# Performance work log

Hardware: AMD Instinct MI355X
Metric: run time of the kernel (lower is better)

Reference implementation:

```python
import jax, jax.numpy as jnp
import numpy as np


def log_g(x):
    # log of g(x) = relu(x)+0.5 for x>=0, sigmoid(x) for x<0 (continuous minGRU activation)
    return jnp.where(x >= 0, jnp.log(jax.nn.relu(x) + 0.5), -jax.nn.softplus(-x))


def parallel_scan_log(log_coeffs, log_values):
    # log_coeffs: [B,T,H], log_values: [B,T+1,H]
    a_star = jnp.pad(jnp.cumsum(log_coeffs, axis=1), ((0, 0), (1, 0), (0, 0)))  # [B,T+1,H]
    log_h = a_star + jax.lax.cumlogsumexp(log_values - a_star, axis=1)
    return jnp.exp(log_h)  # [B,T+1,H]


def setup_inputs() -> dict:
    key = jax.random.key(0)
    B, T, D, H = 8, 4096, 1024, 1024
    k1, k2, k3, k4, k5, k6 = jax.random.split(key, 6)
    scale = 1.0 / np.sqrt(D)
    return {
        "x": jax.random.normal(k1, (B, T, D), dtype=jnp.float32),
        "h_0": jax.random.uniform(k2, (B, 1, H), dtype=jnp.float32),
        "W_z": jax.random.uniform(k3, (H, D), minval=-scale, maxval=scale, dtype=jnp.float32),
        "b_z": jax.random.uniform(k4, (H,), minval=-scale, maxval=scale, dtype=jnp.float32),
        "W_h": jax.random.uniform(k5, (H, D), minval=-scale, maxval=scale, dtype=jnp.float32),
        "b_h": jax.random.uniform(k6, (H,), minval=-scale, maxval=scale, dtype=jnp.float32),
    }


def reference(x, h_0, W_z, b_z, W_h, b_h):
    # k = linear_z(x)
    k = jnp.einsum('btd,hd->bth', x, W_z) + b_z                 # [B,T,H]
    log_z = -jax.nn.softplus(-k)                                # log sigmoid(k)
    log_coeffs = -jax.nn.softplus(k)                            # log (1 - sigmoid(k))
    log_h_0 = log_g(h_0)                                        # [B,1,H]
    log_tilde_h = log_g(jnp.einsum('btd,hd->bth', x, W_h) + b_h)  # [B,T,H]
    log_values = jnp.concatenate([log_h_0, log_z + log_tilde_h], axis=1)  # [B,T+1,H]
    h = parallel_scan_log(log_coeffs, log_values)               # [B,T+1,H]
    return h
```

## Files before the change

kernel.cpp:

```cpp
#include <hip/hip_runtime.h>
#include <stdint.h>

#define B_ 8
#define T_ 4096
#define D_ 1024
#define H_ 1024
#define M_ (B_*T_)
#define K_ D_
#define N_ H_
#define TC 32
#define NC (T_/TC)

typedef short short8 __attribute__((ext_vector_type(8)));
typedef float f32x4 __attribute__((ext_vector_type(4)));
typedef unsigned short ushort8v __attribute__((ext_vector_type(8)));

__device__ __forceinline__ float bf2f(unsigned short u) {
    union { unsigned int i; float f; } x; x.i = ((unsigned int)u) << 16; return x.f;
}
__device__ __forceinline__ unsigned short f2bf(float f) {
    union { float f; unsigned int i; } x; x.f = f;
    unsigned int u = x.i;
    unsigned int r = u + 0x7fffu + ((u >> 16) & 1u);
    return (unsigned short)(r >> 16);
}
__device__ __forceinline__ void gld_lds16(const unsigned short* g, unsigned short* l) {
    __builtin_amdgcn_global_load_lds(
        (const __attribute__((address_space(1))) void*)(const void*)g,
        (__attribute__((address_space(3))) void*)(void*)l, 16, 0, 0);
}
__device__ __forceinline__ float gfun(float x) {
    return x >= 0.f ? x + 0.5f : 1.f / (1.f + __expf(-x));
}

__global__ void cvt_kernel(const float* __restrict__ src, unsigned short* __restrict__ dst, int n4) {
    int i = blockIdx.x * blockDim.x + threadIdx.x;
    const int stride = gridDim.x * blockDim.x;
    for (; i < n4; i += stride) {
        float4 v = ((const float4*)src)[i];
        ushort4 o;
        o.x = f2bf(v.x); o.y = f2bf(v.y); o.z = f2bf(v.z); o.w = f2bf(v.w);
        ((ushort4*)dst)[i] = o;
    }
}

__global__ void cvtw_kernel(const float* __restrict__ Wz, const float* __restrict__ Wh,
                            unsigned short* __restrict__ wzb, unsigned short* __restrict__ whb, int n4) {
    const float* src = blockIdx.y ? Wh : Wz;
    unsigned short* dst = blockIdx.y ? whb : wzb;
    int i = blockIdx.x * blockDim.x + threadIdx.x;
    const int stride = gridDim.x * blockDim.x;
    for (; i < n4; i += stride) {
        float4 v = ((const float4*)src)[i];
        ushort4 o;
        o.x = f2bf(v.x); o.y = f2bf(v.y); o.z = f2bf(v.z); o.w = f2bf(v.w);
        ((ushort4*)dst)[i] = o;
    }
}

#define SB() __builtin_amdgcn_sched_barrier(0)
#define BAR() do { SB(); __builtin_amdgcn_s_barrier(); SB(); } while (0)

__global__ __launch_bounds__(512, 2) void gemm_kernel(
    const unsigned short* __restrict__ Xb,
    const unsigned short* __restrict__ Wzb,
    const unsigned short* __restrict__ Whb,
    const float* __restrict__ bz, const float* __restrict__ bh,
    unsigned short* __restrict__ KzOut, unsigned short* __restrict__ KhOut)
{
    __shared__ __align__(16) unsigned short ldsA[2][256 * 64];
    __shared__ __align__(16) unsigned short ldsB[2][256 * 64];

    const int bx = blockIdx.x;
    const int bn = blockIdx.y;
    const int mat = blockIdx.z;
    const unsigned short* Wb = mat ? Whb : Wzb;
    const float* bias = mat ? bh : bz;
    unsigned short* Out = mat ? KhOut : KzOut;

    const int tid = threadIdx.x;
    const int w = tid >> 6, lane = tid & 63;
    const int wm = w >> 2, wn = w & 3;

    const int srow = lane >> 3;
    const int schunk = ((lane & 7) ^ srow) << 3;
    const unsigned short* gA = Xb + (size_t)(bx * 1024 + srow) * K_ + schunk;
    const unsigned short* gB = Wb + (size_t)(bn * 256 + srow) * K_ + schunk;

#define STAGE_A(s, g, h) do { \
    gld_lds16(gA + (size_t)(((g) >> 4) * 256 + (h)*128 + w*8) * K_ + ((g)&15) * 64, \
              &ldsA[s][((h)*128 + w*8) * 64]); \
    gld_lds16(gA + (size_t)(((g) >> 4) * 256 + (h)*128 + 64 + w*8) * K_ + ((g)&15) * 64, \
              &ldsA[s][((h)*128 + 64 + w*8) * 64]); \
  } while (0)
#define STAGE_B(s, g, h) do { \
    gld_lds16(gB + (size_t)((h)*128 + w*8) * K_ + ((g)&15) * 64, \
              &ldsB[s][((h)*128 + w*8) * 64]); \
    gld_lds16(gB + (size_t)((h)*128 + 64 + w*8) * K_ + ((g)&15) * 64, \
              &ldsB[s][((h)*128 + 64 + w*8) * 64]); \
  } while (0)

    const int lrow = lane & 15;
    const int q = lane >> 4;
    const int sw0 = (q ^ (lane & 7)) << 3;

#define LDA(s, fm, kh) (*(const short8*)&ldsA[s][(wm*128 + (fm)*16 + lrow) * 64 + (sw0 ^ ((kh)*32))])
#define LDB(s, fn, kh) (*(const short8*)&ldsB[s][(wn*64  + (fn)*16 + lrow) * 64 + (sw0 ^ ((kh)*32))])

#define RD_A4(s, fmb) do { \
    _Pragma("unroll") for (int f = 0; f < 4; ++f) { Ar[f][0] = LDA(s, (fmb)+f, 0); Ar[f][1] = LDA(s, (fmb)+f, 1); } \
  } while (0)
#define RD_B2(s, fnb) do { \
    _Pragma("unroll") for (int g2_ = 0; g2_ < 2; ++g2_) { Br[(fnb)+g2_][0] = LDB(s, (fnb)+g2_, 0); Br[(fnb)+g2_][1] = LDB(s, (fnb)+g2_, 1); } \
  } while (0)

#define QUAD(mb, nb) do { \
    __builtin_amdgcn_s_setprio(1); \
    _Pragma("unroll") for (int f = 0; f < 4; ++f) { \
      _Pragma("unroll") for (int g2_ = 0; g2_ < 2; ++g2_) { \
        acc[(mb)+f][(nb)+g2_] = __builtin_amdgcn_mfma_f32_16x16x32_bf16(Ar[f][0], Br[(nb)+g2_][0], acc[(mb)+f][(nb)+g2_], 0, 0, 0); \
        acc[(mb)+f][(nb)+g2_] = __builtin_amdgcn_mfma_f32_16x16x32_bf16(Ar[f][1], Br[(nb)+g2_][1], acc[(mb)+f][(nb)+g2_], 0, 0, 0); \
      } \
    } \
    __builtin_amdgcn_s_setprio(0); \
  } while (0)

    f32x4 acc[8][4];
    short8 Ar[4][2], Br[4][2];

    float bb[4];
#pragma unroll
    for (int fn = 0; fn < 4; ++fn) bb[fn] = bias[bn * 256 + wn * 64 + fn * 16 + lrow];

    STAGE_B(0, 0, 0); STAGE_B(0, 0, 1);
    STAGE_A(0, 0, 0); STAGE_A(0, 0, 1);
    STAGE_B(1, 1, 0); STAGE_B(1, 1, 1);
    SB();
    asm volatile("s_waitcnt vmcnt(4)" ::: "memory");
    BAR();

#pragma unroll 1
    for (int t = 0; t < 4; ++t) {
#pragma unroll
        for (int i = 0; i < 8; ++i)
#pragma unroll
            for (int j = 0; j < 4; ++j) acc[i][j] = (f32x4){0.f, 0.f, 0.f, 0.f};

#pragma unroll 1
        for (int i = 0; i < 8; ++i) {
            const int g1 = t * 16 + 2 * i + 1;
            const int g2 = g1 + 1;
            const int g3 = g1 + 2;
            const bool st = (g2 < 64);

            RD_A4(0, 0); RD_B2(0, 0);
            STAGE_A(1, g1, 0);
            BAR();
            QUAD(0, 0);
            BAR();
            RD_B2(0, 2);
            STAGE_A(1, g1, 1);
            BAR();
            QUAD(0, 2);
            BAR();
            RD_A4(0, 4);
            if (st) STAGE_B(0, g2, 0);
            BAR();
            QUAD(4, 0);
            BAR();
            if (st) {
                STAGE_B(0, g2, 1);
                SB();
                asm volatile("s_waitcnt vmcnt(4)" ::: "memory");
            } else {
                asm volatile("s_waitcnt vmcnt(0)" ::: "memory");
            }
            BAR();
            QUAD(4, 2);
            BAR();
            RD_A4(1, 0); RD_B2(1, 0);
            if (st) STAGE_A(0, g2, 0);
            BAR();
            QUAD(0, 0);
            BAR();
            RD_B2(1, 2);
            if (st) STAGE_A(0, g2, 1);
            BAR();
            QUAD(0, 2);
            BAR();
            RD_A4(1, 4);
            if (st) STAGE_B(1, g3, 0);
            BAR();
            QUAD(4, 0);
            BAR();
            if (st) {
                STAGE_B(1, g3, 1);
                SB();
                asm volatile("s_waitcnt vmcnt(4)" ::: "memory");
            }
            BAR();
            QUAD(4, 2);
            BAR();
        }

#pragma unroll
        for (int fn = 0; fn < 4; ++fn) {
            const int n = bn * 256 + wn * 64 + fn * 16 + lrow;
#pragma unroll
            for (int fm = 0; fm < 8; ++fm) {
                const int mq = (bx * 4 + t) * 64 + wm * 32 + fm * 4 + q;
                ushort4 o;
                o.x = f2bf(acc[fm][fn][0] + bb[fn]);
                o.y = f2bf(acc[fm][fn][1] + bb[fn]);
                o.z = f2bf(acc[fm][fn][2] + bb[fn]);
                o.w = f2bf(acc[fm][fn][3] + bb[fn]);
                *(ushort4*)(Out + ((size_t)mq * N_ + n) * 4) = o;
            }
        }
    }
}


__global__ __launch_bounds__(256) void scanA_kernel(const unsigned short* __restrict__ Kz,
                                                    const unsigned short* __restrict__ Kh,
                                                    float* __restrict__ Fc, float* __restrict__ Vc)
{
    const int c = blockIdx.x, b = blockIdx.y;
    const int hb = threadIdx.x * 4;
    float F[4] = {1.f, 1.f, 1.f, 1.f}, V[4] = {0.f, 0.f, 0.f, 0.f};
    size_t base = ((size_t)(b * (T_ / 4) + c * (TC / 4)) * N_ + hb) * 4;
    for (int qq = 0; qq < TC / 4; qq++) {
        ushort8v z0 = *(const ushort8v*)(Kz + base);
        ushort8v z1 = *(const ushort8v*)(Kz + base + 8);
        ushort8v h0v = *(const ushort8v*)(Kh + base);
        ushort8v h1v = *(const ushort8v*)(Kh + base + 8);
        base += (size_t)N_ * 4;
#pragma unroll
        for (int r = 0; r < 4; r++) {
            float kzf[4] = {bf2f(z0[r]), bf2f(z0[4 + r]), bf2f(z1[r]), bf2f(z1[4 + r])};
            float khf[4] = {bf2f(h0v[r]), bf2f(h0v[4 + r]), bf2f(h1v[r]), bf2f(h1v[4 + r])};
#pragma unroll
            for (int j = 0; j < 4; j++) {
                float f = 1.f / (1.f + __expf(kzf[j]));
                float v = (1.f - f) * gfun(khf[j]);
                V[j] = f * V[j] + v;
                F[j] *= f;
            }
        }
    }
    size_t o = ((size_t)(b * NC + c)) * H_ + hb;
    *(float4*)(Fc + o) = make_float4(F[0], F[1], F[2], F[3]);
    *(float4*)(Vc + o) = make_float4(V[0], V[1], V[2], V[3]);
}

__global__ __launch_bounds__(64) void scanB_kernel(const float* __restrict__ h0,
                                                   const float* __restrict__ Fc,
                                                   const float* __restrict__ Vc,
                                                   float* __restrict__ Carry,
                                                   float* __restrict__ Out)
{
    const int b = blockIdx.x;
    const int h = blockIdx.y * 256 + threadIdx.x * 4;
    float cy[4];
#pragma unroll
    for (int j = 0; j < 4; j++) cy[j] = gfun(h0[(size_t)b * H_ + h + j]);
    *(float4*)(Out + (size_t)b * (T_ + 1) * H_ + h) = make_float4(cy[0], cy[1], cy[2], cy[3]);
    size_t o = ((size_t)(b * NC)) * H_ + h;
    float4 F4 = *(const float4*)(Fc + o);
    float4 V4 = *(const float4*)(Vc + o);
    for (int c = 0; c < NC; c++) {
        const size_t on = o + H_;
        float4 nF, nV;
        if (c + 1 < NC) {
            nF = *(const float4*)(Fc + on);
            nV = *(const float4*)(Vc + on);
        }
        *(float4*)(Carry + o) = make_float4(cy[0], cy[1], cy[2], cy[3]);
        cy[0] = F4.x * cy[0] + V4.x;
        cy[1] = F4.y * cy[1] + V4.y;
        cy[2] = F4.z * cy[2] + V4.z;
        cy[3] = F4.w * cy[3] + V4.w;
        F4 = nF; V4 = nV; o = on;
    }
}

__global__ __launch_bounds__(256) void scanC_kernel(const unsigned short* __restrict__ Kz,
                                                    const unsigned short* __restrict__ Kh,
                                                    const float* __restrict__ Carry,
                                                    float* __restrict__ Out)
{
    const int c = blockIdx.x, b = blockIdx.y;
    const int hb = threadIdx.x * 4;
    float cy[4];
    {
        float4 c4 = *(const float4*)(Carry + ((size_t)(b * NC + c)) * H_ + hb);
        cy[0] = c4.x; cy[1] = c4.y; cy[2] = c4.z; cy[3] = c4.w;
    }
    size_t base = ((size_t)(b * (T_ / 4) + c * (TC / 4)) * N_ + hb) * 4;
    size_t ob = ((size_t)(b * (T_ + 1) + c * TC + 1)) * H_ + hb;
    for (int qq = 0; qq < TC / 4; qq++) {
        ushort8v z0 = *(const ushort8v*)(Kz + base);
        ushort8v z1 = *(const ushort8v*)(Kz + base + 8);
        ushort8v h0v = *(const ushort8v*)(Kh + base);
        ushort8v h1v = *(const ushort8v*)(Kh + base + 8);
        base += (size_t)N_ * 4;
#pragma unroll
        for (int r = 0; r < 4; r++) {
            float kzf[4] = {bf2f(z0[r]), bf2f(z0[4 + r]), bf2f(z1[r]), bf2f(z1[4 + r])};
            float khf[4] = {bf2f(h0v[r]), bf2f(h0v[4 + r]), bf2f(h1v[r]), bf2f(h1v[4 + r])};
#pragma unroll
            for (int j = 0; j < 4; j++) {
                float f = 1.f / (1.f + __expf(kzf[j]));
                float v = (1.f - f) * gfun(khf[j]);
                cy[j] = f * cy[j] + v;
            }
            *(float4*)(Out + ob) = make_float4(cy[0], cy[1], cy[2], cy[3]);
            ob += H_;
        }
    }
}

extern "C" void kernel_launch(void* const* d_in, const int* in_sizes, int n_in,
                              void* d_out, int out_size, void* d_ws, size_t ws_size,
                              hipStream_t stream)
{
    const float* x  = (const float*)d_in[0];
    const float* h0 = (const float*)d_in[1];
    const float* Wz = (const float*)d_in[2];
    const float* bz = (const float*)d_in[3];
    const float* Wh = (const float*)d_in[4];
    const float* bh = (const float*)d_in[5];
    float* out = (float*)d_out;

    char* ws = (char*)d_ws;
    unsigned short* xb  = (unsigned short*)ws; ws += (size_t)M_ * K_ * 2;
    unsigned short* wzb = (unsigned short*)ws; ws += (size_t)N_ * K_ * 2;
    unsigned short* whb = (unsigned short*)ws; ws += (size_t)N_ * K_ * 2;
    unsigned short* kz  = (unsigned short*)ws; ws += (size_t)M_ * N_ * 2;
    unsigned short* kh  = (unsigned short*)ws; ws += (size_t)M_ * N_ * 2;
    float* Fc    = (float*)ws; ws += (size_t)B_ * NC * H_ * 4;
    float* Vc    = (float*)ws; ws += (size_t)B_ * NC * H_ * 4;
    float* Carry = (float*)ws; ws += (size_t)B_ * NC * H_ * 4;

    cvt_kernel<<<2048, 256, 0, stream>>>(x, xb, M_ * K_ / 4);
    cvtw_kernel<<<dim3(128, 2), 256, 0, stream>>>(Wz, Wh, wzb, whb, N_ * K_ / 4);

    dim3 gg(M_ / 1024, N_ / 256, 2);
    gemm_kernel<<<gg, 512, 0, stream>>>(xb, wzb, whb, bz, bh, kz, kh);

    scanA_kernel<<<dim3(NC, B_), 256, 0, stream>>>(kz, kh, Fc, Vc);
    scanB_kernel<<<dim3(B_, H_ / 256), 64, 0, stream>>>(h0, Fc, Vc, Carry, out);
    scanC_kernel<<<dim3(NC, B_), 256, 0, stream>>>(kz, kh, Carry, out);
}
```

Measured before the change: 459.7 us.

## Fuse three-pass chunked scan into single decoupled-lookback scan kernel

Replaces the separate chunk-reduce, serial carry, and chunk-apply scan kernels with one kernel using decoupled lookback. Each block publishes its aggregate and then its inclusive prefix through per-chunk flags, and spins on its predecessors. The chunk size is doubled, to 64. This removes two kernel launches and the slow serial carry kernel. In exchange it adds spin-wait synchronisation whose progress relies on lower block indices being scheduled first, plus a flag-clear launch.

```diff
diff --git a/kernel.cpp b/kernel.cpp
--- a/kernel.cpp
+++ b/kernel.cpp
@@ -8,8 +8,8 @@
 #define M_ (B_*T_)
 #define K_ D_
 #define N_ H_
-#define TC 32
-#define NC (T_/TC)
+#define TC2 64
+#define NC2 (T_/TC2)
 
 typedef short short8 __attribute__((ext_vector_type(8)));
 typedef float f32x4 __attribute__((ext_vector_type(4)));
@@ -58,6 +58,11 @@
     }
 }
 
+__global__ void clear_kernel(int* __restrict__ flags, int n) {
+    int i = blockIdx.x * blockDim.x + threadIdx.x;
+    if (i < n) flags[i] = 0;
+}
+
 #define SB() __builtin_amdgcn_sched_barrier(0)
 #define BAR() do { SB(); __builtin_amdgcn_s_barrier(); SB(); } while (0)
 
@@ -221,15 +226,20 @@
 }
 
 
-__global__ __launch_bounds__(256) void scanA_kernel(const unsigned short* __restrict__ Kz,
-                                                    const unsigned short* __restrict__ Kh,
-                                                    float* __restrict__ Fc, float* __restrict__ Vc)
+__global__ __launch_bounds__(256) void scan_fused(
+    const unsigned short* __restrict__ Kz, const unsigned short* __restrict__ Kh,
+    const float* __restrict__ h0,
+    float* __restrict__ FA, float* __restrict__ VA, float* __restrict__ Incl,
+    int* flags, float* __restrict__ Out)
 {
     const int c = blockIdx.x, b = blockIdx.y;
     const int hb = threadIdx.x * 4;
+    __shared__ int sh_flag;
+
     float F[4] = {1.f, 1.f, 1.f, 1.f}, V[4] = {0.f, 0.f, 0.f, 0.f};
-    size_t base = ((size_t)(b * (T_ / 4) + c * (TC / 4)) * N_ + hb) * 4;
-    for (int qq = 0; qq < TC / 4; qq++) {
+    const size_t base0 = ((size_t)(b * (T_ / 4) + c * (TC2 / 4)) * N_ + hb) * 4;
+    size_t base = base0;
+    for (int qq = 0; qq < TC2 / 4; qq++) {
         ushort8v z0 = *(const ushort8v*)(Kz + base);
         ushort8v z1 = *(const ushort8v*)(Kz + base + 8);
         ushort8v h0v = *(const ushort8v*)(Kh + base);
@@ -248,57 +258,73 @@
             }
         }
     }
-    size_t o = ((size_t)(b * NC + c)) * H_ + hb;
-    *(float4*)(Fc + o) = make_float4(F[0], F[1], F[2], F[3]);
-    *(float4*)(Vc + o) = make_float4(V[0], V[1], V[2], V[3]);
-}
-
-__global__ __launch_bounds__(64) void scanB_kernel(const float* __restrict__ h0,
-                                                   const float* __restrict__ Fc,
-                                                   const float* __restrict__ Vc,
-                                                   float* __restrict__ Carry,
-                                                   float* __restrict__ Out)
-{
-    const int b = blockIdx.x;
-    const int h = blockIdx.y * 256 + threadIdx.x * 4;
+
+    const size_t oc = ((size_t)(b * NC2 + c)) * H_ + hb;
+    *(float4*)(FA + oc) = make_float4(F[0], F[1], F[2], F[3]);
+    *(float4*)(VA + oc) = make_float4(V[0], V[1], V[2], V[3]);
+    __threadfence();
+    __syncthreads();
+    if (threadIdx.x == 0)
+        __hip_atomic_store(&flags[b * NC2 + c], 1, __ATOMIC_RELEASE, __HIP_MEMORY_SCOPE_AGENT);
+
+    float aF[4] = {1.f, 1.f, 1.f, 1.f}, aV[4] = {0.f, 0.f, 0.f, 0.f};
     float cy[4];
-#pragma unroll
-    for (int j = 0; j < 4; j++) cy[j] = gfun(h0[(size_t)b * H_ + h + j]);
-    *(float4*)(Out + (size_t)b * (T_ + 1) * H_ + h) = make_float4(cy[0], cy[1], cy[2], cy[3]);
-    size_t o = ((size_t)(b * NC)) * H_ + h;
-    float4 F4 = *(const float4*)(Fc + o);
-    float4 V4 = *(const float4*)(Vc + o);
-    for (int c = 0; c < NC; c++) {
-        const size_t on = o + H_;
-        float4 nF, nV;
-        if (c + 1 < NC) {
-            nF = *(const float4*)(Fc + on);
-            nV = *(const float4*)(Vc + on);
-        }
-        *(float4*)(Carry + o) = make_float4(cy[0], cy[1], cy[2], cy[3]);
-        cy[0] = F4.x * cy[0] + V4.x;
-        cy[1] = F4.y * cy[1] + V4.y;
-        cy[2] = F4.z * cy[2] + V4.z;
-        cy[3] = F4.w * cy[3] + V4.w;
-        F4 = nF; V4 = nV; o = on;
-    }
-}
-
-__global__ __launch_bounds__(256) void scanC_kernel(const unsigned short* __restrict__ Kz,
-                                                    const unsigned short* __restrict__ Kh,
-                                                    const float* __restrict__ Carry,
-                                                    float* __restrict__ Out)
-{
-    const int c = blockIdx.x, b = blockIdx.y;
-    const int hb = threadIdx.x * 4;
-    float cy[4];
+    bool done = false;
+    int j = c - 1;
+    while (!done && j >= 0) {
+        if (threadIdx.x == 0) {
+            int s;
+            while ((s = __hip_atomic_load(&flags[b * NC2 + j], __ATOMIC_ACQUIRE,
+                                          __HIP_MEMORY_SCOPE_AGENT)) == 0)
+                __builtin_amdgcn_s_sleep(8);
+            sh_flag = s;
+        }
+        __syncthreads();
+        const int s = sh_flag;
+        __syncthreads();
+        const size_t oj = ((size_t)(b * NC2 + j)) * H_ + hb;
+        if (s == 2) {
+            float4 I = *(const float4*)(Incl + oj);
+            cy[0] = aF[0] * I.x + aV[0];
+            cy[1] = aF[1] * I.y + aV[1];
+            cy[2] = aF[2] * I.z + aV[2];
+            cy[3] = aF[3] * I.w + aV[3];
+            done = true;
+        } else {
+            float4 fj = *(const float4*)(FA + oj);
+            float4 vj = *(const float4*)(VA + oj);
+            aV[0] = aF[0] * vj.x + aV[0];  aF[0] *= fj.x;
+            aV[1] = aF[1] * vj.y + aV[1];  aF[1] *= fj.y;
+            aV[2] = aF[2] * vj.z + aV[2];  aF[2] *= fj.z;
+            aV[3] = aF[3] * vj.w + aV[3];  aF[3] *= fj.w;
+            --j;
+        }
+    }
+    if (!done) {
+#pragma unroll
+        for (int k = 0; k < 4; ++k)
+            cy[k] = aF[k] * gfun(h0[(size_t)b * H_ + hb + k]) + aV[k];
+    }
+
     {
-        float4 c4 = *(const float4*)(Carry + ((size_t)(b * NC + c)) * H_ + hb);
-        cy[0] = c4.x; cy[1] = c4.y; cy[2] = c4.z; cy[3] = c4.w;
-    }
-    size_t base = ((size_t)(b * (T_ / 4) + c * (TC / 4)) * N_ + hb) * 4;
-    size_t ob = ((size_t)(b * (T_ + 1) + c * TC + 1)) * H_ + hb;
-    for (int qq = 0; qq < TC / 4; qq++) {
+        float4 inc = make_float4(F[0] * cy[0] + V[0], F[1] * cy[1] + V[1],
+                                 F[2] * cy[2] + V[2], F[3] * cy[3] + V[3]);
+        *(float4*)(Incl + oc) = inc;
+    }
+    __threadfence();
+    __syncthreads();
+    if (threadIdx.x == 0)
+        __hip_atomic_store(&flags[b * NC2 + c], 2, __ATOMIC_RELEASE, __HIP_MEMORY_SCOPE_AGENT);
+
+    if (c == 0) {
+        float4 r0 = make_float4(gfun(h0[(size_t)b * H_ + hb + 0]), gfun(h0[(size_t)b * H_ + hb + 1]),
+                                gfun(h0[(size_t)b * H_ + hb + 2]), gfun(h0[(size_t)b * H_ + hb + 3]));
+        *(float4*)(Out + (size_t)b * (T_ + 1) * H_ + hb) = r0;
+    }
+
+    base = base0;
+    size_t ob = ((size_t)(b * (T_ + 1) + c * TC2 + 1)) * H_ + hb;
+    for (int qq = 0; qq < TC2 / 4; qq++) {
         ushort8v z0 = *(const ushort8v*)(Kz + base);
         ushort8v z1 = *(const ushort8v*)(Kz + base + 8);
         ushort8v h0v = *(const ushort8v*)(Kh + base);
@@ -309,10 +335,10 @@
             float kzf[4] = {bf2f(z0[r]), bf2f(z0[4 + r]), bf2f(z1[r]), bf2f(z1[4 + r])};
             float khf[4] = {bf2f(h0v[r]), bf2f(h0v[4 + r]), bf2f(h1v[r]), bf2f(h1v[4 + r])};
 #pragma unroll
-            for (int j = 0; j < 4; j++) {
-                float f = 1.f / (1.f + __expf(kzf[j]));
-                float v = (1.f - f) * gfun(khf[j]);
-                cy[j] = f * cy[j] + v;
+            for (int jj = 0; jj < 4; jj++) {
+                float f = 1.f / (1.f + __expf(kzf[jj]));
+                float v = (1.f - f) * gfun(khf[jj]);
+                cy[jj] = f * cy[jj] + v;
             }
             *(float4*)(Out + ob) = make_float4(cy[0], cy[1], cy[2], cy[3]);
             ob += H_;
@@ -338,17 +364,17 @@
     unsigned short* whb = (unsigned short*)ws; ws += (size_t)N_ * K_ * 2;
     unsigned short* kz  = (unsigned short*)ws; ws += (size_t)M_ * N_ * 2;
     unsigned short* kh  = (unsigned short*)ws; ws += (size_t)M_ * N_ * 2;
-    float* Fc    = (float*)ws; ws += (size_t)B_ * NC * H_ * 4;
-    float* Vc    = (float*)ws; ws += (size_t)B_ * NC * H_ * 4;
-    float* Carry = (float*)ws; ws += (size_t)B_ * NC * H_ * 4;
-
+    float* FA   = (float*)ws; ws += (size_t)B_ * NC2 * H_ * 4;
+    float* VA   = (float*)ws; ws += (size_t)B_ * NC2 * H_ * 4;
+    float* Incl = (float*)ws; ws += (size_t)B_ * NC2 * H_ * 4;
+    int* flags  = (int*)ws;   ws += 4096;
+
+    clear_kernel<<<1, 512, 0, stream>>>(flags, B_ * NC2);
     cvt_kernel<<<2048, 256, 0, stream>>>(x, xb, M_ * K_ / 4);
     cvtw_kernel<<<dim3(128, 2), 256, 0, stream>>>(Wz, Wh, wzb, whb, N_ * K_ / 4);
 
     dim3 gg(M_ / 1024, N_ / 256, 2);
     gemm_kernel<<<gg, 512, 0, stream>>>(xb, wzb, whb, bz, bh, kz, kh);
 
-    scanA_kernel<<<dim3(NC, B_), 256, 0, stream>>>(kz, kh, Fc, Vc);
-    scanB_kernel<<<dim3(B_, H_ / 256), 64, 0, stream>>>(h0, Fc, Vc, Carry, out);
-    scanC_kernel<<<dim3(NC, B_), 256, 0, stream>>>(kz, kh, Carry, out);
-}
+    scan_fused<<<dim3(NC2, B_), 256, 0, stream>>>(kz, kh, h0, FA, VA, Incl, flags, out);
+}
```

New measurement: 654.3 us. 42.3% more time.
